# Kernel tuning notes

Hardware: AMD Instinct MI355X
Metric: run time of the kernel (lower is better)

The kernel has to match this reference:

```python
import jax, jax.numpy as jnp
import numpy as np

N = 50000
E = 600000
IN = 128
H = 4
F = 32  # per-head out; concat output = H*F = 128
NEG_SLOPE = 0.2


def setup_inputs() -> dict:
    key = jax.random.key(0)
    k1, k2, k3, k4, k5, k6 = jax.random.split(key, 6)
    x = jax.random.normal(k1, (N, IN), dtype=jnp.float32)
    edge_index = jax.random.randint(k2, (2, E), 0, N, dtype=jnp.int64)
    W = jax.random.normal(k3, (IN, H * F), dtype=jnp.float32) * 0.05
    att_src = jax.random.normal(k4, (H, F), dtype=jnp.float32) * 0.05
    att_dst = jax.random.normal(k5, (H, F), dtype=jnp.float32) * 0.05
    bias = jnp.zeros((H * F,), dtype=jnp.float32)
    return {"x": x, "edge_index": edge_index, "W": W,
            "att_src": att_src, "att_dst": att_dst, "bias": bias}


def reference(x, edge_index, W, att_src, att_dst, bias):
    n = x.shape[0]
    # add self loops (PyG GATConv default)
    loop = jnp.arange(n, dtype=edge_index.dtype)
    src = jnp.concatenate([edge_index[0], loop])
    dst = jnp.concatenate([edge_index[1], loop])

    h = (x @ W).reshape(n, H, F)                      # [N,H,F]
    a_s = jnp.einsum('nhf,hf->nh', h, att_src)        # [N,H]
    a_d = jnp.einsum('nhf,hf->nh', h, att_dst)        # [N,H]

    e = a_s[src] + a_d[dst]                           # [E',H]
    e = jax.nn.leaky_relu(e, NEG_SLOPE)
    # segment softmax over incoming edges of each destination node
    m = jax.ops.segment_max(e, dst, num_segments=n)   # [N,H]
    m = jnp.where(jnp.isfinite(m), m, 0.0)
    ex = jnp.exp(e - m[dst])                          # [E',H]
    denom = jax.ops.segment_sum(ex, dst, num_segments=n)  # [N,H]
    alpha = ex / denom[dst]                           # [E',H]

    msgs = alpha[:, :, None] * h[src]                 # [E',H,F]
    out = jax.ops.segment_sum(msgs, dst, num_segments=n)  # [N,H,F]
    out = out.reshape(n, H * F) + bias
    return jax.nn.relu(out)
```

## Files before the change

kernel.cpp:

```cpp
#include <hip/hip_runtime.h>

#define NEG_SLOPE 0.2f
#define CAP 64
#define NB 256
#define MAXB 4096
#define A_EDGES 2048
#define A_BLOCKS 293
#define GEMM_BLOCKS 782

typedef __attribute__((ext_vector_type(8))) short short8;
typedef __attribute__((ext_vector_type(4))) float f32x4;

__device__ __forceinline__ unsigned short f2bf(float f) {
    union { float f; unsigned int i; } v; v.f = f;
    unsigned int r = v.i + 0x7FFF + ((v.i >> 16) & 1);
    return (unsigned short)(r >> 16);
}
__device__ __forceinline__ float lrelu(float v) {
    return v > 0.f ? v : NEG_SLOPE * v;
}

__global__ void gat_prep(const float* __restrict__ W,
                         const float* __restrict__ att_src,
                         const float* __restrict__ att_dst,
                         unsigned short* __restrict__ wt,
                         int* __restrict__ bcur)
{
    int i = blockIdx.x * blockDim.x + threadIdx.x;
    if (i < NB) bcur[i] = 0;
    if (i >= 144 * 128) return;
    int r = i >> 7, k = i & 127;
    float v = 0.f;
    if (r < 128) {
        v = W[k * 128 + r];
    } else if (r < 136) {
        int hh = (r - 128) & 3;
        const float* att = (r < 132) ? att_src : att_dst;
        float s = 0.f;
        #pragma unroll 8
        for (int f = 0; f < 32; f++)
            s = fmaf(W[k * 128 + hh * 32 + f], att[hh * 32 + f], s);
        v = s;
    }
    wt[i] = f2bf(v);
}

__global__ __launch_bounds__(256) void gat_mega(
    const float* __restrict__ x, const unsigned short* __restrict__ wt,
    const int* __restrict__ ei, unsigned short* __restrict__ hb,
    float* __restrict__ a_s, float* __restrict__ a_d,
    int* __restrict__ bcur, unsigned int* __restrict__ bbuf, int nE, int n)
{
    const int bid = blockIdx.x;
    if (bid < A_BLOCKS) {
        __shared__ int hist[NB];
        __shared__ int gbase[NB];
        const int tid = threadIdx.x;
        hist[tid] = 0;
        __syncthreads();

        int base = bid * A_EDGES + tid * 8;
        int sreg[8], dreg[8], rreg[8];
        bool act = (base + 8 <= nE);
        if (act) {
            int4 s0 = ((const int4*)(ei + base))[0];
            int4 s1 = ((const int4*)(ei + base))[1];
            int4 d0 = ((const int4*)(ei + nE + base))[0];
            int4 d1 = ((const int4*)(ei + nE + base))[1];
            sreg[0]=s0.x; sreg[1]=s0.y; sreg[2]=s0.z; sreg[3]=s0.w;
            sreg[4]=s1.x; sreg[5]=s1.y; sreg[6]=s1.z; sreg[7]=s1.w;
            dreg[0]=d0.x; dreg[1]=d0.y; dreg[2]=d0.z; dreg[3]=d0.w;
            dreg[4]=d1.x; dreg[5]=d1.y; dreg[6]=d1.z; dreg[7]=d1.w;
            #pragma unroll
            for (int j = 0; j < 8; j++)
                rreg[j] = atomicAdd(&hist[dreg[j] >> 8], 1);
        }
        __syncthreads();
        {
            int h = hist[tid];
            gbase[tid] = (h > 0) ? atomicAdd(&bcur[tid], h) : 0;
        }
        __syncthreads();
        if (act) {
            #pragma unroll
            for (int j = 0; j < 8; j++) {
                int b = dreg[j] >> 8;
                int idx = gbase[b] + rreg[j];
                if (idx < MAXB)
                    bbuf[(size_t)b * MAXB + idx] =
                        ((unsigned int)dreg[j] << 16) | (unsigned int)sreg[j];
            }
        }
        return;
    }
    const int wave = threadIdx.x >> 6, lane = threadIdx.x & 63;
    const int quad = lane >> 4, l15 = lane & 15;
    const int m0 = (bid - A_BLOCKS) * 64 + wave * 16;
    if (m0 >= n) return;
    const int row = m0 + l15;

    f32x4 acc[9];
    #pragma unroll
    for (int t = 0; t < 9; t++) acc[t] = (f32x4){0.f, 0.f, 0.f, 0.f};

    const float* xr = x + (size_t)row * 128 + quad * 8;
    #pragma unroll
    for (int kk = 0; kk < 4; ++kk) {
        float4 f0 = ((const float4*)(xr + kk * 32))[0];
        float4 f1 = ((const float4*)(xr + kk * 32))[1];
        short8 afrag;
        afrag[0] = (short)f2bf(f0.x); afrag[1] = (short)f2bf(f0.y);
        afrag[2] = (short)f2bf(f0.z); afrag[3] = (short)f2bf(f0.w);
        afrag[4] = (short)f2bf(f1.x); afrag[5] = (short)f2bf(f1.y);
        afrag[6] = (short)f2bf(f1.z); afrag[7] = (short)f2bf(f1.w);
        #pragma unroll
        for (int t = 0; t < 9; ++t) {
            short8 bfrag = *(const short8*)(wt + (size_t)(t * 16 + l15) * 128 + kk * 32 + quad * 8);
            acc[t] = __builtin_amdgcn_mfma_f32_16x16x32_bf16(afrag, bfrag, acc[t], 0, 0, 0);
        }
    }

    #pragma unroll
    for (int t = 0; t < 8; ++t)
        #pragma unroll
        for (int r = 0; r < 4; ++r) {
            int orow = m0 + quad * 4 + r;
            hb[(size_t)orow * 128 + t * 16 + l15] = f2bf(acc[t][r]);
        }
    if (l15 < 8) {
        float* dst = (l15 < 4) ? a_s : a_d;
        int hh = l15 & 3;
        #pragma unroll
        for (int r = 0; r < 4; ++r) {
            int orow = m0 + quad * 4 + r;
            dst[(size_t)orow * 4 + hh] = acc[8][r];
        }
    }
}

__global__ __launch_bounds__(512) void gat_ell_build(
    const int* __restrict__ bcur, const unsigned int* __restrict__ bbuf,
    unsigned short* __restrict__ csr, int* __restrict__ cnt, int n)
{
    __shared__ int lcnt[NB];
    const int b = blockIdx.x, tid = threadIdx.x;
    if (tid < NB) lcnt[tid] = 0;
    __syncthreads();
    int count = min(bcur[b], MAXB);
    for (int i = tid; i < count; i += 512) {
        unsigned int u = bbuf[(size_t)b * MAXB + i];
        int d = (int)(u >> 16);
        int slot = atomicAdd(&lcnt[d & 255], 1);
        if (slot < CAP)
            csr[(size_t)d * CAP + slot] = (unsigned short)(u & 0xFFFFu);
    }
    __syncthreads();
    if (tid < NB) {
        int d = (b << 8) + tid;
        if (d < n) cnt[d] = lcnt[tid];
    }
}

__global__ __launch_bounds__(256) void gat_accumulate(
    const int* __restrict__ cnt, const unsigned short* __restrict__ csr,
    const float4* __restrict__ a_s4, const float4* __restrict__ a_d4,
    const uint4* __restrict__ h4, const float* __restrict__ bias,
    float* __restrict__ out, int n)
{
    __shared__ float wtab[4][256];
    __shared__ int   stab[4][64];
    int lane = threadIdx.x & 63;
    int wslot = threadIdx.x >> 6;
    int d = blockIdx.x * 4 + wslot;
    if (d >= n) return;

    int deg  = min(cnt[d], CAP - 1);
    int degi = deg + 1;
    int slotv = (lane < deg) ? (int)csr[(size_t)d * CAP + lane] : d;
    stab[wslot][lane] = slotv;

    float4 ad = a_d4[d];
    float4 w4 = {0.f, 0.f, 0.f, 0.f};
    if (lane < degi) {
        float4 as = a_s4[slotv];
        w4.x = __expf(lrelu(as.x + ad.x));
        w4.y = __expf(lrelu(as.y + ad.y));
        w4.z = __expf(lrelu(as.z + ad.z));
        w4.w = __expf(lrelu(as.w + ad.w));
    }
    ((float4*)wtab[wslot])[lane] = w4;

    int quad = lane >> 4, c = lane & 15;
    int head = c >> 2;
    const float* wrow = wtab[wslot];
    const int*   srow = stab[wslot];

    float acc[8] = {0.f,0.f,0.f,0.f,0.f,0.f,0.f,0.f};
    float den = 0.f;

    for (int j = 0; j < degi; j += 16) {
        int je[4]; int sv[4]; uint4 hv[4];
        #pragma unroll
        for (int u = 0; u < 4; u++) {
            je[u] = j + 4 * u + quad;
            sv[u] = srow[je[u]];
        }
        #pragma unroll
        for (int u = 0; u < 4; u++)
            if (je[u] < degi)
                hv[u] = h4[(size_t)sv[u] * 16 + c];
        #pragma unroll
        for (int u = 0; u < 4; u++) {
            if (je[u] < degi) {
                float w = wrow[je[u] * 4 + head];
                union { unsigned int i; float f; } lo, hi;
                #pragma unroll
                for (int k = 0; k < 4; k++) {
                    unsigned int uu = (&hv[u].x)[k];
                    lo.i = uu << 16; hi.i = uu & 0xFFFF0000u;
                    acc[2*k]   = fmaf(w, lo.f, acc[2*k]);
                    acc[2*k+1] = fmaf(w, hi.f, acc[2*k+1]);
                }
                den += w;
            }
        }
    }

    #pragma unroll
    for (int m = 16; m <= 32; m <<= 1) {
        #pragma unroll
        for (int k = 0; k < 8; k++) acc[k] += __shfl_xor(acc[k], m);
        den += __shfl_xor(den, m);
    }

    if (quad == 0) {
        float inv = 1.f / den;
        float4 b0 = ((const float4*)bias)[2*c];
        float4 b1 = ((const float4*)bias)[2*c + 1];
        float4 o0, o1;
        o0.x = fmaxf(acc[0]*inv + b0.x, 0.f); o0.y = fmaxf(acc[1]*inv + b0.y, 0.f);
        o0.z = fmaxf(acc[2]*inv + b0.z, 0.f); o0.w = fmaxf(acc[3]*inv + b0.w, 0.f);
        o1.x = fmaxf(acc[4]*inv + b1.x, 0.f); o1.y = fmaxf(acc[5]*inv + b1.y, 0.f);
        o1.z = fmaxf(acc[6]*inv + b1.z, 0.f); o1.w = fmaxf(acc[7]*inv + b1.w, 0.f);
        ((float4*)out)[(size_t)d * 32 + 2*c]     = o0;
        ((float4*)out)[(size_t)d * 32 + 2*c + 1] = o1;
    }
}

extern "C" void kernel_launch(void* const* d_in, const int* in_sizes, int n_in,
                              void* d_out, int out_size, void* d_ws, size_t ws_size,
                              hipStream_t stream)
{
    const float* x       = (const float*)d_in[0];
    const int*   ei      = (const int*)d_in[1];
    const float* W       = (const float*)d_in[2];
    const float* att_src = (const float*)d_in[3];
    const float* att_dst = (const float*)d_in[4];
    const float* bias    = (const float*)d_in[5];

    const int n  = in_sizes[0] / 128;
    const int nE = in_sizes[1] / 2;

    char* wsb = (char*)d_ws;
    unsigned short* hb  = (unsigned short*)wsb;
    unsigned short* wt  = hb + (size_t)n * 128;
    float* a_s = (float*)(wt + 144 * 128);
    float* a_d = a_s + (size_t)n * 4;
    int*   cnt  = (int*)(a_d + (size_t)n * 4);
    int*   bcur = cnt + n;
    unsigned short* csr = (unsigned short*)(bcur + NB);
    unsigned int*  bbuf = (unsigned int*)(csr + (size_t)n * CAP);
    float* out = (float*)d_out;

    const int nbkt = (n + 255) >> 8;

    gat_prep<<<(144 * 128 + 255) / 256, 256, 0, stream>>>(W, att_src, att_dst,
                                                          wt, bcur);
    gat_mega<<<A_BLOCKS + GEMM_BLOCKS, 256, 0, stream>>>(x, wt, ei, hb, a_s,
                                                         a_d, bcur, bbuf, nE, n);
    gat_ell_build<<<nbkt, 512, 0, stream>>>(bcur, bbuf, csr, cnt, n);
    gat_accumulate<<<(n + 3) / 4, 256, 0, stream>>>(cnt, csr, (const float4*)a_s,
                                                    (const float4*)a_d,
                                                    (const uint4*)hb, bias, out, n);
}
```

Baseline: 150.5 us.

## Stage GAT weight matrix in swizzled LDS and vectorize ELL bucket build

The GEMM blocks of the mega kernel now copy the whole bf16 weight matrix (plus attention columns) into XOR-swizzled shared memory and read MFMA B-fragments from LDS instead of global memory. They also prefetch all x row data into registers before the MFMA loop, and the histogram blocks reuse the same shared buffer. The ELL build kernel uses 1024 threads, each loading four bucket entries with one 128-bit load. The cost is about 36KB of LDS per block, which may limit occupancy, plus a per-block weight copy and barrier.

```diff
diff --git a/kernel.cpp b/kernel.cpp
--- a/kernel.cpp
+++ b/kernel.cpp
@@ -45,16 +45,17 @@
     wt[i] = f2bf(v);
 }
 
-__global__ __launch_bounds__(256) void gat_mega(
+__global__ __launch_bounds__(256, 2) void gat_mega(
     const float* __restrict__ x, const unsigned short* __restrict__ wt,
     const int* __restrict__ ei, unsigned short* __restrict__ hb,
     float* __restrict__ a_s, float* __restrict__ a_d,
     int* __restrict__ bcur, unsigned int* __restrict__ bbuf, int nE, int n)
 {
+    __shared__ unsigned short wlds[144 * 128];
     const int bid = blockIdx.x;
     if (bid < A_BLOCKS) {
-        __shared__ int hist[NB];
-        __shared__ int gbase[NB];
+        int* hist  = (int*)wlds;
+        int* gbase = hist + NB;
         const int tid = threadIdx.x;
         hist[tid] = 0;
         __syncthreads();
@@ -93,29 +94,48 @@
         }
         return;
     }
-    const int wave = threadIdx.x >> 6, lane = threadIdx.x & 63;
+    const int tid = threadIdx.x;
+    #pragma unroll
+    for (int j = 0; j < 9; j++) {
+        int i = tid + j * 256;
+        int row = i >> 4, s = i & 15;
+        int sp = s ^ (row & 7);
+        *(short8*)(wlds + row * 128 + sp * 8) = *(const short8*)(wt + (size_t)i * 8);
+    }
+    __syncthreads();
+
+    const int wave = tid >> 6, lane = tid & 63;
     const int quad = lane >> 4, l15 = lane & 15;
+    const int xm = l15 & 7;
     const int m0 = (bid - A_BLOCKS) * 64 + wave * 16;
     if (m0 >= n) return;
     const int row = m0 + l15;
 
+    const float* xr = x + (size_t)row * 128 + quad * 8;
+    float4 xa[8];
+    #pragma unroll
+    for (int kk = 0; kk < 4; ++kk) {
+        xa[2*kk]   = ((const float4*)(xr + kk * 32))[0];
+        xa[2*kk+1] = ((const float4*)(xr + kk * 32))[1];
+    }
+
     f32x4 acc[9];
     #pragma unroll
     for (int t = 0; t < 9; t++) acc[t] = (f32x4){0.f, 0.f, 0.f, 0.f};
 
-    const float* xr = x + (size_t)row * 128 + quad * 8;
     #pragma unroll
     for (int kk = 0; kk < 4; ++kk) {
-        float4 f0 = ((const float4*)(xr + kk * 32))[0];
-        float4 f1 = ((const float4*)(xr + kk * 32))[1];
+        float4 f0 = xa[2*kk], f1 = xa[2*kk+1];
         short8 afrag;
         afrag[0] = (short)f2bf(f0.x); afrag[1] = (short)f2bf(f0.y);
         afrag[2] = (short)f2bf(f0.z); afrag[3] = (short)f2bf(f0.w);
         afrag[4] = (short)f2bf(f1.x); afrag[5] = (short)f2bf(f1.y);
         afrag[6] = (short)f2bf(f1.z); afrag[7] = (short)f2bf(f1.w);
+        const int sl = (kk * 4 + quad);
         #pragma unroll
         for (int t = 0; t < 9; ++t) {
-            short8 bfrag = *(const short8*)(wt + (size_t)(t * 16 + l15) * 128 + kk * 32 + quad * 8);
+            short8 bfrag = *(const short8*)(wlds + (size_t)(t * 16 + l15) * 128
+                                            + ((sl ^ xm) << 3));
             acc[t] = __builtin_amdgcn_mfma_f32_16x16x32_bf16(afrag, bfrag, acc[t], 0, 0, 0);
         }
     }
@@ -138,7 +158,7 @@
     }
 }
 
-__global__ __launch_bounds__(512) void gat_ell_build(
+__global__ __launch_bounds__(1024) void gat_ell_build(
     const int* __restrict__ bcur, const unsigned int* __restrict__ bbuf,
     unsigned short* __restrict__ csr, int* __restrict__ cnt, int n)
 {
@@ -147,12 +167,20 @@
     if (tid < NB) lcnt[tid] = 0;
     __syncthreads();
     int count = min(bcur[b], MAXB);
-    for (int i = tid; i < count; i += 512) {
-        unsigned int u = bbuf[(size_t)b * MAXB + i];
-        int d = (int)(u >> 16);
-        int slot = atomicAdd(&lcnt[d & 255], 1);
-        if (slot < CAP)
-            csr[(size_t)d * CAP + slot] = (unsigned short)(u & 0xFFFFu);
+    int i = tid * 4;
+    if (i < count) {
+        uint4 u4 = ((const uint4*)(bbuf + (size_t)b * MAXB))[tid];
+        unsigned int uu[4] = {u4.x, u4.y, u4.z, u4.w};
+        #pragma unroll
+        for (int j = 0; j < 4; j++) {
+            if (i + j < count) {
+                unsigned int u = uu[j];
+                int d = (int)(u >> 16);
+                int slot = atomicAdd(&lcnt[d & 255], 1);
+                if (slot < CAP)
+                    csr[(size_t)d * CAP + slot] = (unsigned short)(u & 0xFFFFu);
+            }
+        }
     }
     __syncthreads();
     if (tid < NB) {
@@ -278,7 +306,7 @@
                                                           wt, bcur);
     gat_mega<<<A_BLOCKS + GEMM_BLOCKS, 256, 0, stream>>>(x, wt, ei, hb, a_s,
                                                          a_d, bcur, bbuf, nE, n);
-    gat_ell_build<<<nbkt, 512, 0, stream>>>(bcur, bbuf, csr, cnt, n);
+    gat_ell_build<<<nbkt, 1024, 0, stream>>>(bcur, bbuf, csr, cnt, n);
     gat_accumulate<<<(n + 3) / 4, 256, 0, stream>>>(cnt, csr, (const float4*)a_s,
                                                     (const float4*)a_d,
                                                     (const uint4*)hb, bias, out, n);
```

New measurement: 136.7 us. -9.2%, faster.
